# Optimization experiments

Hardware: AMD Instinct MI355X
Metric: run time of the kernel (lower is better)

Reference implementation:

```python
import jax, jax.numpy as jnp
import numpy as np

N = 50000          # nodes
E = 800000         # edges (avg degree 16)
F_IN = 64          # node feature dim
F_EDGE = 8         # edge feature dim (carried through, unused by EdgeConv)
DIMS = [64, 64, 64, 8]   # hidden layers + final num_classes layer (no BN)
EPS = 1e-5


def mish(x):
    return x * jnp.tanh(jax.nn.softplus(x))


def _init_layer(key, din, dout):
    k1, k2, k3, k4 = jax.random.split(key, 4)
    s1 = 1.0 / np.sqrt(2 * din)
    s2 = 1.0 / np.sqrt(dout)
    w1 = jax.random.uniform(k1, (2 * din, dout), jnp.float32, -s1, s1)
    b1 = jax.random.uniform(k2, (dout,), jnp.float32, -s1, s1)
    w2 = jax.random.uniform(k3, (dout, dout), jnp.float32, -s2, s2)
    b2 = jax.random.uniform(k4, (dout,), jnp.float32, -s2, s2)
    return w1, b1, w2, b2


def setup_inputs() -> dict:
    key = jax.random.key(0)
    ks = jax.random.split(key, 8)
    inp = {
        "x": jax.random.normal(ks[0], (N, F_IN), jnp.float32),
        "edge_index": jax.random.randint(ks[1], (2, E), 0, N, jnp.int32),
        "edge_attr": jax.random.normal(ks[2], (E, F_EDGE), jnp.float32),
    }
    din = F_IN
    for l, dout in enumerate(DIMS):
        w1, b1, w2, b2 = _init_layer(jax.random.fold_in(ks[3], l), din, dout)
        inp[f"w1_{l}"] = w1
        inp[f"b1_{l}"] = b1
        inp[f"w2_{l}"] = w2
        inp[f"b2_{l}"] = b2
        if l < len(DIMS) - 1:  # BN on all but final classifier layer
            inp[f"g_{l}"] = jnp.ones((dout,), jnp.float32)
            inp[f"be_{l}"] = jnp.zeros((dout,), jnp.float32)
        din = dout
    return inp


def _forward(x, edge_index, params):
    src = edge_index[0]
    dst = edge_index[1]
    for (w1, b1, w2, b2, g, be) in params:
        xi = x[dst]                       # [E, din] target feats
        xj = x[src]                       # [E, din] source feats
        m = jnp.concatenate([xi, xj - xi], axis=-1)   # [E, 2*din]
        h = mish(m @ w1 + b1) @ w2 + b2               # [E, dout]
        agg = jax.ops.segment_max(h, dst, num_segments=N)
        x = jnp.where(jnp.isfinite(agg), agg, 0.0)    # empty segments -> 0
        if g is not None:                 # BatchNorm1d, batch stats (train fwd)
            mu = x.mean(axis=0)
            var = x.var(axis=0)
            x = (x - mu) * jax.lax.rsqrt(var + EPS) * g + be
    return x


def reference(x, edge_index, edge_attr,
              w1_0, b1_0, w2_0, b2_0, g_0, be_0,
              w1_1, b1_1, w2_1, b2_1, g_1, be_1,
              w1_2, b1_2, w2_2, b2_2, g_2, be_2,
              w1_3, b1_3, w2_3, b2_3):
    params = [
        (w1_0, b1_0, w2_0, b2_0, g_0, be_0),
        (w1_1, b1_1, w2_1, b2_1, g_1, be_1),
        (w1_2, b1_2, w2_2, b2_2, g_2, be_2),
        (w1_3, b1_3, w2_3, b2_3, None, None),
    ]
    return _forward(x, edge_index, params)
```

## Files before the change

### kernel.cpp

```cpp
#include <hip/hip_runtime.h>
#include <hip/hip_bf16.h>
#include <math.h>

#define NN 50000
#define EE 800000
#define NT (EE / 16)
#define NBLK 1408
#define CHT 9

typedef short s8v __attribute__((ext_vector_type(8)));
typedef float f4v __attribute__((ext_vector_type(4)));

__device__ __forceinline__ short f2bf(float f) {
    unsigned u = __float_as_uint(f);
    u += 0x7fffu + ((u >> 16) & 1u);
    return (short)(u >> 16);
}

__device__ __forceinline__ unsigned enc(float f) {
    unsigned u = __float_as_uint(f);
    return (u & 0x80000000u) ? ~u : (u | 0x80000000u);
}
__device__ __forceinline__ float dec(unsigned k) {
    if (k == 0u) return 0.0f;
    unsigned u = (k & 0x80000000u) ? (k & 0x7fffffffu) : ~k;
    return __uint_as_float(u);
}

__device__ __forceinline__ float mish_fast(float v) {
    float t = __expf(v);
    float s = t * (t + 2.0f);
    float r = v * s * __builtin_amdgcn_rcpf(s + 2.0f);
    return (v > 15.0f) ? v : r;
}

#define MFMA16(a, b, c) __builtin_amdgcn_mfma_f32_16x16x32_bf16(a, b, c, 0, 0, 0)


__global__ __launch_bounds__(256) void count_k(const int* __restrict__ ei,
                                               int* __restrict__ cnt) {
    int e = blockIdx.x * 256 + threadIdx.x;
    if (e < EE) atomicAdd(&cnt[ei[EE + e]], 1);
}

#define NBS 196

__global__ __launch_bounds__(256) void scan_part(const int* __restrict__ cnt,
                                                 int* __restrict__ part) {
    int t = threadIdx.x, i = blockIdx.x * 256 + t;
    __shared__ int ps[256];
    ps[t] = (i < NN) ? cnt[i] : 0;
    __syncthreads();
    for (int off = 128; off > 0; off >>= 1) {
        if (t < off) ps[t] += ps[t + off];
        __syncthreads();
    }
    if (t == 0) part[blockIdx.x] = ps[0];
}

__global__ __launch_bounds__(256) void scan_top(int* __restrict__ part) {
    int t = threadIdx.x;
    int v = (t < NBS) ? part[t] : 0;
    __shared__ int ps[256];
    ps[t] = v;
    __syncthreads();
    for (int off = 1; off < 256; off <<= 1) {
        int u = (t >= off) ? ps[t - off] : 0;
        __syncthreads();
        ps[t] += u;
        __syncthreads();
    }
    if (t < NBS) part[t] = ps[t] - v;
}

__global__ __launch_bounds__(256) void scan_fin(const int* __restrict__ cnt,
                                                const int* __restrict__ part,
                                                int* __restrict__ row_off,
                                                int* __restrict__ cur) {
    int t = threadIdx.x, i = blockIdx.x * 256 + t;
    int v = (i < NN) ? cnt[i] : 0;
    __shared__ int ps[256];
    ps[t] = v;
    __syncthreads();
    for (int off = 1; off < 256; off <<= 1) {
        int u = (t >= off) ? ps[t - off] : 0;
        __syncthreads();
        ps[t] += u;
        __syncthreads();
    }
    int excl = ps[t] - v + part[blockIdx.x];
    if (i < NN) {
        row_off[i] = excl;
        cur[i] = excl;
        if (i == NN - 1) row_off[NN] = excl + v;
    }
}

__global__ __launch_bounds__(256) void scatter_k(const int* __restrict__ ei,
                                                 int* __restrict__ cur,
                                                 int* __restrict__ csr_src,
                                                 int* __restrict__ csr_dst) {
    int e = blockIdx.x * 256 + threadIdx.x;
    if (e < EE) {
        int d = ei[EE + e];
        int p = atomicAdd(&cur[d], 1);
        csr_src[p] = ei[e];
        csr_dst[p] = d;
    }
}


__global__ __launch_bounds__(256)
void cvt_bf16(const float* __restrict__ x, unsigned short* __restrict__ xb, int n) {
    int i = blockIdx.x * 256 + threadIdx.x;
    if (i < n) xb[i] = (unsigned short)f2bf(x[i]);
}


__global__ __launch_bounds__(256)
void a0_mfma(const unsigned short* __restrict__ xb, const float* __restrict__ w1,
             const float* __restrict__ b1, float* __restrict__ a0, int nwt) {
    const int lane = threadIdx.x & 63;
    const int wid = blockIdx.x * 4 + (threadIdx.x >> 6);
    const int i = lane & 15, q = lane >> 4;
    s8v wf[4][2];
#pragma unroll
    for (int nb = 0; nb < 4; nb++)
#pragma unroll
        for (int kh = 0; kh < 2; kh++)
#pragma unroll
            for (int j = 0; j < 8; j++) {
                int k = kh * 32 + q * 8 + j, n = nb * 16 + i;
                wf[nb][kh][j] = f2bf(w1[k * 64 + n] - w1[(64 + k) * 64 + n]);
            }
    float bia[4];
#pragma unroll
    for (int nb = 0; nb < 4; nb++) bia[nb] = b1[nb * 16 + i];

    const int ntiles = NN / 16;
    for (int t = wid; t < ntiles; t += nwt) {
        const int row0 = t * 16;
        const unsigned short* xr = xb + (size_t)(row0 + i) * 64;
        s8v af0 = *(const s8v*)(xr + q * 8);
        s8v af1 = *(const s8v*)(xr + 32 + q * 8);
        const int rowq = row0 + q * 4;
#pragma unroll
        for (int nb = 0; nb < 4; nb++) {
            f4v c = {0.f, 0.f, 0.f, 0.f};
            c = MFMA16(af0, wf[nb][0], c);
            c = MFMA16(af1, wf[nb][1], c);
#pragma unroll
            for (int r = 0; r < 4; r++)
                a0[(size_t)(rowq + r) * 64 + i * 4 + nb] = c[r] + bia[nb];
        }
    }
}


__global__ __launch_bounds__(256)
void a0_mfma8(const unsigned short* __restrict__ xb, const float* __restrict__ w1,
              const float* __restrict__ b1, float* __restrict__ a0, int nwt) {
    const int lane = threadIdx.x & 63;
    const int wid = blockIdx.x * 4 + (threadIdx.x >> 6);
    const int i = lane & 15, q = lane >> 4;
    s8v wf[2];
#pragma unroll
    for (int kh = 0; kh < 2; kh++)
#pragma unroll
        for (int j = 0; j < 8; j++) {
            int k = kh * 32 + q * 8 + j;
            wf[kh][j] = (i < 8) ? f2bf(w1[k * 8 + i] - w1[(64 + k) * 8 + i]) : (short)0;
        }
    const float bia = (i < 8) ? b1[i] : 0.0f;

    const int ntiles = NN / 16;
    for (int t = wid; t < ntiles; t += nwt) {
        const int row0 = t * 16;
        const unsigned short* xr = xb + (size_t)(row0 + i) * 64;
        s8v af0 = *(const s8v*)(xr + q * 8);
        s8v af1 = *(const s8v*)(xr + 32 + q * 8);
        f4v c = {0.f, 0.f, 0.f, 0.f};
        c = MFMA16(af0, wf[0], c);
        c = MFMA16(af1, wf[1], c);
        if (i < 8) {
            const int rowq = row0 + q * 4;
#pragma unroll
            for (int r = 0; r < 4; r++)
                a0[(size_t)(rowq + r) * 8 + i] = c[r] + bia;
        }
    }
}


__global__ __launch_bounds__(256)
void edge_mfma64(const unsigned short* __restrict__ xb, const float* __restrict__ a0,
                 const float* __restrict__ w1, const float* __restrict__ w2,
                 const float* __restrict__ b2,
                 const int* __restrict__ csr_src, const int* __restrict__ csr_dst,
                 unsigned* __restrict__ y) {
    __shared__ float uld[4][16 * 68];
    __shared__ int dseg[4][2][20];
    __shared__ short w2l[8 * 64 * 8];
    const int lane = threadIdx.x & 63;
    const int wv = threadIdx.x >> 6;
    const int wid = blockIdx.x * 4 + wv;
    const int i = lane & 15, q = lane >> 4;
    float* up = &uld[wv][0];

    s8v w1f[4][2];
#pragma unroll
    for (int nb = 0; nb < 4; nb++)
#pragma unroll
        for (int kh = 0; kh < 2; kh++)
#pragma unroll
            for (int j = 0; j < 8; j++) {
                int k = kh * 32 + q * 8 + j, n = nb * 16 + i;
                w1f[nb][kh][j] = f2bf(w1[(64 + k) * 64 + n]);
            }
    {
        const int nb = wv;
#pragma unroll
        for (int kh = 0; kh < 2; kh++) {
            s8v uu;
#pragma unroll
            for (int j = 0; j < 8; j++) {
                int k = kh * 32 + q * 8 + j;
                uu[j] = f2bf(w2[k * 64 + nb * 16 + i]);
            }
            *(s8v*)(w2l + ((nb * 2 + kh) * 64 + lane) * 8) = uu;
        }
    }
    __syncthreads();

    const float b2c = b2[lane];

    int t = wid * CHT;
    if (t >= NT) return;
    const int tend = (t + CHT < NT) ? (t + CHT) : NT;

    s8v af0_c, af1_c;
    {
        int s0 = csr_src[t * 16 + i];
        const unsigned short* xr = xb + (size_t)s0 * 64;
        af0_c = *(const s8v*)(xr + q * 8);
        af1_c = *(const s8v*)(xr + 32 + q * 8);
    }
    int src_n = (t + 1 < tend) ? csr_src[(t + 1) * 16 + i] : 0;
    if (lane < 17) {
        int e = t * 16 + lane;
        dseg[wv][t & 1][lane] = (e < EE) ? csr_dst[e] : -1;
    }
    asm volatile("s_waitcnt lgkmcnt(0)" ::: "memory");
    int dq_c[4];
#pragma unroll
    for (int r = 0; r < 4; r++) dq_c[r] = dseg[wv][t & 1][q * 4 + r];
    f4v a0r_c[4];
#pragma unroll
    for (int r = 0; r < 4; r++)
        a0r_c[r] = *(const f4v*)(a0 + (size_t)dq_c[r] * 64 + i * 4);

    float run = -INFINITY;

    for (; t < tend; t++) {
        const bool has_n = (t + 1) < tend;
        int* dsg = &dseg[wv][t & 1][0];
        int* dsg_n = &dseg[wv][(t + 1) & 1][0];

        if (has_n && lane < 17) {
            int e = (t + 1) * 16 + lane;
            dsg_n[lane] = (e < EE) ? csr_dst[e] : -1;
        }
        s8v af0_n = {0,0,0,0,0,0,0,0}, af1_n = {0,0,0,0,0,0,0,0};
        if (has_n) {
            const unsigned short* xr = xb + (size_t)src_n * 64;
            af0_n = *(const s8v*)(xr + q * 8);
            af1_n = *(const s8v*)(xr + 32 + q * 8);
        }
        int src_nn = (t + 2 < tend) ? csr_src[(t + 2) * 16 + i] : 0;

        f4v c0 = {0.f, 0.f, 0.f, 0.f}, c1 = c0, c2 = c0, c3 = c0;
        c0 = MFMA16(af0_c, w1f[0][0], c0); c0 = MFMA16(af1_c, w1f[0][1], c0);
        c1 = MFMA16(af0_c, w1f[1][0], c1); c1 = MFMA16(af1_c, w1f[1][1], c1);
        c2 = MFMA16(af0_c, w1f[2][0], c2); c2 = MFMA16(af1_c, w1f[2][1], c2);
        c3 = MFMA16(af0_c, w1f[3][0], c3); c3 = MFMA16(af1_c, w1f[3][1], c3);

        asm volatile("" ::: "memory");
#pragma unroll
        for (int r = 0; r < 4; r++) {
            const int ro = (q * 4 + r) * 68 + i;
            up[ro +  0] = mish_fast(c0[r] + a0r_c[r][0]);
            up[ro + 16] = mish_fast(c1[r] + a0r_c[r][1]);
            up[ro + 32] = mish_fast(c2[r] + a0r_c[r][2]);
            up[ro + 48] = mish_fast(c3[r] + a0r_c[r][3]);
        }
        asm volatile("s_waitcnt lgkmcnt(0)" ::: "memory");

        int dq_n[4];
        f4v a0r_n[4];
        if (has_n) {
#pragma unroll
            for (int r = 0; r < 4; r++) dq_n[r] = dsg_n[q * 4 + r];
#pragma unroll
            for (int r = 0; r < 4; r++)
                a0r_n[r] = *(const f4v*)(a0 + (size_t)dq_n[r] * 64 + i * 4);
        }

        s8v uf[2];
#pragma unroll
        for (int kh = 0; kh < 2; kh++) {
            const f4v* rp = (const f4v*)(up + i * 68 + kh * 32 + q * 8);
            f4v v0 = rp[0], v1 = rp[1];
            s8v uu;
            uu[0] = f2bf(v0[0]); uu[1] = f2bf(v0[1]);
            uu[2] = f2bf(v0[2]); uu[3] = f2bf(v0[3]);
            uu[4] = f2bf(v1[0]); uu[5] = f2bf(v1[1]);
            uu[6] = f2bf(v1[2]); uu[7] = f2bf(v1[3]);
            uf[kh] = uu;
        }
        asm volatile("" ::: "memory");

        f4v cc[4];
#pragma unroll
        for (int nb = 0; nb < 4; nb++) {
            s8v b0 = *(const s8v*)(w2l + ((nb * 2 + 0) * 64 + lane) * 8);
            s8v b1v = *(const s8v*)(w2l + ((nb * 2 + 1) * 64 + lane) * 8);
            f4v c = {0.f, 0.f, 0.f, 0.f};
            c = MFMA16(uf[0], b0, c);
            c = MFMA16(uf[1], b1v, c);
            cc[nb] = c;
        }

#pragma unroll
        for (int nb = 0; nb < 4; nb++)
#pragma unroll
            for (int r = 0; r < 4; r++)
                up[(q * 4 + r) * 68 + nb * 16 + i] = cc[nb][r];
        asm volatile("s_waitcnt lgkmcnt(0)" ::: "memory");

        float v[16];
#pragma unroll
        for (int row = 0; row < 16; row++) v[row] = up[row * 68 + lane];

        int dcur = dsg[0];
#pragma unroll
        for (int row = 0; row < 16; row++) {
            run = fmaxf(run, v[row]);
            int dn = (row < 15) ? dsg[row + 1] : (has_n ? dsg[16] : -1);
            if (dcur != dn) {
                atomicMax(&y[(size_t)dcur * 64 + lane], enc(run + b2c));
                run = -INFINITY;
            }
            dcur = dn;
        }
        asm volatile("s_waitcnt lgkmcnt(0)" ::: "memory");

        src_n = src_nn;
        af0_c = af0_n; af1_c = af1_n;
#pragma unroll
        for (int r = 0; r < 4; r++) a0r_c[r] = a0r_n[r];
    }
}


__global__ __launch_bounds__(256)
void edge_mfma16(const unsigned short* __restrict__ xb, const float* __restrict__ a0,
                 const float* __restrict__ w1, const float* __restrict__ w2,
                 const float* __restrict__ b2,
                 const int* __restrict__ csr_src, const int* __restrict__ csr_dst,
                 unsigned* __restrict__ y8) {
    __shared__ float uld[4][16 * 20];
    __shared__ int dseg[4][2][20];
    const int lane = threadIdx.x & 63;
    const int wv = threadIdx.x >> 6;
    const int wid = blockIdx.x * 4 + wv;
    const int i = lane & 15, q = lane >> 4;
    float* up = &uld[wv][0];

    s8v w1f[2], w2f;
#pragma unroll
    for (int kh = 0; kh < 2; kh++)
#pragma unroll
        for (int j = 0; j < 8; j++) {
            int k = kh * 32 + q * 8 + j;
            w1f[kh][j] = (i < 8) ? f2bf(w1[(64 + k) * 8 + i]) : (short)0;
        }
#pragma unroll
    for (int j = 0; j < 8; j++)
        w2f[j] = (q == 0 && i < 8) ? f2bf(w2[j * 8 + i]) : (short)0;
    const float b2c = (lane < 8) ? b2[lane] : 0.0f;

    int t = wid * CHT;
    if (t >= NT) return;
    const int tend = (t + CHT < NT) ? (t + CHT) : NT;

    s8v af0_c, af1_c;
    {
        int s0 = csr_src[t * 16 + i];
        const unsigned short* xr = xb + (size_t)s0 * 64;
        af0_c = *(const s8v*)(xr + q * 8);
        af1_c = *(const s8v*)(xr + 32 + q * 8);
    }
    int src_n = (t + 1 < tend) ? csr_src[(t + 1) * 16 + i] : 0;
    if (lane < 17) {
        int e = t * 16 + lane;
        dseg[wv][t & 1][lane] = (e < EE) ? csr_dst[e] : -1;
    }
    asm volatile("s_waitcnt lgkmcnt(0)" ::: "memory");
    int dq_c[4];
#pragma unroll
    for (int r = 0; r < 4; r++) dq_c[r] = dseg[wv][t & 1][q * 4 + r];
    float av_c[4];
#pragma unroll
    for (int r = 0; r < 4; r++)
        av_c[r] = (i < 8) ? a0[(size_t)dq_c[r] * 8 + i] : 0.0f;

    float run = -INFINITY;

    for (; t < tend; t++) {
        const bool has_n = (t + 1) < tend;
        int* dsg = &dseg[wv][t & 1][0];
        int* dsg_n = &dseg[wv][(t + 1) & 1][0];

        if (has_n && lane < 17) {
            int e = (t + 1) * 16 + lane;
            dsg_n[lane] = (e < EE) ? csr_dst[e] : -1;
        }
        s8v af0_n = {0,0,0,0,0,0,0,0}, af1_n = {0,0,0,0,0,0,0,0};
        if (has_n) {
            const unsigned short* xr = xb + (size_t)src_n * 64;
            af0_n = *(const s8v*)(xr + q * 8);
            af1_n = *(const s8v*)(xr + 32 + q * 8);
        }
        int src_nn = (t + 2 < tend) ? csr_src[(t + 2) * 16 + i] : 0;

        f4v c = {0.f, 0.f, 0.f, 0.f};
        c = MFMA16(af0_c, w1f[0], c);
        c = MFMA16(af1_c, w1f[1], c);

        asm volatile("" ::: "memory");
#pragma unroll
        for (int r = 0; r < 4; r++)
            up[(q * 4 + r) * 20 + i] = mish_fast(c[r] + av_c[r]);
        asm volatile("s_waitcnt lgkmcnt(0)" ::: "memory");

        int dq_n[4];
        float av_n[4] = {0, 0, 0, 0};
        if (has_n) {
#pragma unroll
            for (int r = 0; r < 4; r++) dq_n[r] = dsg_n[q * 4 + r];
#pragma unroll
            for (int r = 0; r < 4; r++)
                av_n[r] = (i < 8) ? a0[(size_t)dq_n[r] * 8 + i] : 0.0f;
        }

        s8v uf = {0,0,0,0,0,0,0,0};
        if (q < 2) {
            const f4v* rp = (const f4v*)(up + i * 20 + q * 8);
            f4v v0 = rp[0], v1 = rp[1];
            uf[0] = f2bf(v0[0]); uf[1] = f2bf(v0[1]);
            uf[2] = f2bf(v0[2]); uf[3] = f2bf(v0[3]);
            uf[4] = f2bf(v1[0]); uf[5] = f2bf(v1[1]);
            uf[6] = f2bf(v1[2]); uf[7] = f2bf(v1[3]);
        }
        asm volatile("" ::: "memory");

        f4v cc = {0.f, 0.f, 0.f, 0.f};
        cc = MFMA16(uf, w2f, cc);

#pragma unroll
        for (int r = 0; r < 4; r++)
            up[(q * 4 + r) * 20 + i] = cc[r];
        asm volatile("s_waitcnt lgkmcnt(0)" ::: "memory");

        float v[16];
#pragma unroll
        for (int row = 0; row < 16; row++) v[row] = up[row * 20 + (lane & 7)];

        int dcur = dsg[0];
#pragma unroll
        for (int row = 0; row < 16; row++) {
            run = fmaxf(run, v[row]);
            int dn = (row < 15) ? dsg[row + 1] : (has_n ? dsg[16] : -1);
            if (dcur != dn) {
                if (lane < 8)
                    atomicMax(&y8[(size_t)dcur * 8 + lane], enc(run + b2c));
                run = -INFINITY;
            }
            dcur = dn;
        }
        asm volatile("s_waitcnt lgkmcnt(0)" ::: "memory");

        src_n = src_nn;
        af0_c = af0_n; af1_c = af1_n;
#pragma unroll
        for (int r = 0; r < 4; r++) av_c[r] = av_n[r];
    }
}


__global__ __launch_bounds__(256)
void bn_stats(const unsigned* __restrict__ yk, float* __restrict__ st) {
    const int tid = threadIdx.x;
    const int ch = tid & 63, grp = tid >> 6;
    float s = 0, qq = 0;
    for (int n = blockIdx.x * 4 + grp; n < NN; n += gridDim.x * 4) {
        float v = dec(yk[(size_t)n * 64 + ch]);
        s += v;
        qq = fmaf(v, v, qq);
    }
    __shared__ float ls[256], lq[256];
    ls[tid] = s; lq[tid] = qq;
    __syncthreads();
    if (tid < 64) {
        s  = ls[tid] + ls[tid + 64] + ls[tid + 128] + ls[tid + 192];
        qq = lq[tid] + lq[tid + 64] + lq[tid + 128] + lq[tid + 192];
        atomicAdd(&st[ch], s);
        atomicAdd(&st[64 + ch], qq);
    }
}

__global__ __launch_bounds__(256)
void bn_apply(unsigned* __restrict__ yk, const float* __restrict__ st,
              const float* __restrict__ g, const float* __restrict__ be,
              unsigned short* __restrict__ xbout) {
    int idx = blockIdx.x * 256 + threadIdx.x;
    if (idx >= NN * 64) return;
    int ch = idx & 63;
    float mu  = st[ch] * (1.0f / NN);
    float var = st[64 + ch] * (1.0f / NN) - mu * mu;
    float sc  = rsqrtf(var + 1e-5f) * g[ch];
    float v = (dec(yk[idx]) - mu) * sc + be[ch];
    xbout[idx] = (unsigned short)f2bf(v);
    yk[idx] = 0u;
}

__global__ __launch_bounds__(256)
void decode_out(const unsigned* __restrict__ y8, float* __restrict__ out) {
    int idx = blockIdx.x * 256 + threadIdx.x;
    if (idx < NN * 8) out[idx] = dec(y8[idx]);
}


extern "C" void kernel_launch(void* const* d_in, const int* in_sizes, int n_in,
                              void* d_out, int out_size, void* d_ws, size_t ws_size,
                              hipStream_t stream) {
    const float* x0 = (const float*)d_in[0];
    const int*   ei = (const int*)d_in[1];
    const float* w1[4] = {(const float*)d_in[3],  (const float*)d_in[9],
                          (const float*)d_in[15], (const float*)d_in[21]};
    const float* b1[4] = {(const float*)d_in[4],  (const float*)d_in[10],
                          (const float*)d_in[16], (const float*)d_in[22]};
    const float* w2[4] = {(const float*)d_in[5],  (const float*)d_in[11],
                          (const float*)d_in[17], (const float*)d_in[23]};
    const float* b2[4] = {(const float*)d_in[6],  (const float*)d_in[12],
                          (const float*)d_in[18], (const float*)d_in[24]};
    const float* gg[3] = {(const float*)d_in[7],  (const float*)d_in[13],
                          (const float*)d_in[19]};
    const float* be[3] = {(const float*)d_in[8],  (const float*)d_in[14],
                          (const float*)d_in[20]};

    char* p = (char*)d_ws;
    auto alloc = [&](size_t bytes) -> char* {
        char* r = p;
        p += (bytes + 255) & ~(size_t)255;
        return r;
    };
    int*      cnt     = (int*)alloc((size_t)NN * 4);
    int*      part    = (int*)alloc((size_t)NBS * 4);
    int*      row_off = (int*)alloc((size_t)(NN + 1) * 4);
    int*      cur     = (int*)alloc((size_t)NN * 4);
    int*      csr_s   = (int*)alloc((size_t)EE * 4);
    int*      csr_d   = (int*)alloc((size_t)EE * 4);
    float*    st      = (float*)alloc(3 * 128 * 4);
    float*    a0      = (float*)alloc((size_t)NN * 64 * 4);
    unsigned* y       = (unsigned*)alloc((size_t)NN * 64 * 4);
    unsigned* y8      = (unsigned*)alloc((size_t)NN * 8 * 4);
    unsigned short* xb0 = (unsigned short*)alloc((size_t)NN * 64 * 2);
    unsigned short* xbA = (unsigned short*)alloc((size_t)NN * 64 * 2);
    unsigned short* xbB = xb0;

    hipMemsetAsync(cnt, 0, (size_t)NN * 4, stream);
    hipMemsetAsync(st, 0, 3 * 128 * 4, stream);
    hipMemsetAsync(y, 0, (size_t)NN * 64 * 4, stream);
    hipMemsetAsync(y8, 0, (size_t)NN * 8 * 4, stream);

    count_k<<<(EE + 255) / 256, 256, 0, stream>>>(ei, cnt);
    scan_part<<<NBS, 256, 0, stream>>>(cnt, part);
    scan_top<<<1, 256, 0, stream>>>(part);
    scan_fin<<<NBS, 256, 0, stream>>>(cnt, part, row_off, cur);
    scatter_k<<<(EE + 255) / 256, 256, 0, stream>>>(ei, cur, csr_s, csr_d);
    cvt_bf16<<<(NN * 64 + 255) / 256, 256, 0, stream>>>(x0, xb0, NN * 64);

    const int NBA = 256;
    const int NWA = NBA * 4;

    const unsigned short* xin[3] = {xb0, xbA, xbB};
    unsigned short* xout[3] = {xbA, xbB, xbA};
    for (int l = 0; l < 3; l++) {
        a0_mfma<<<NBA, 256, 0, stream>>>(xin[l], w1[l], b1[l], a0, NWA);
        edge_mfma64<<<NBLK, 256, 0, stream>>>(xin[l], a0, w1[l], w2[l], b2[l],
                                              csr_s, csr_d, y);
        bn_stats<<<256, 256, 0, stream>>>(y, st + 128 * l);
        bn_apply<<<(NN * 64 + 255) / 256, 256, 0, stream>>>(y, st + 128 * l,
                                                            gg[l], be[l], xout[l]);
    }

    a0_mfma8<<<NBA, 256, 0, stream>>>(xbA, w1[3], b1[3], a0, NWA);
    edge_mfma16<<<NBLK, 256, 0, stream>>>(xbA, a0, w1[3], w2[3], b2[3],
                                          csr_s, csr_d, y8);
    decode_out<<<(NN * 8 + 255) / 256, 256, 0, stream>>>(y8, (float*)d_out);
}
```

Baseline: 547.6 us.

## Fuse BN apply with next-layer node projection and bf16 conversion

Merges the float-to-bf16 conversion with the first per-node projection kernel, and folds the y/y8 zeroing into it instead of using memsets. It also merges the BatchNorm apply step with the next layer's node-side MFMA projection, so normalized features feed the projection directly from registers. This removes several kernel launches and an extra read and write of the bf16 node features per layer. In exchange each fused kernel does more work per tile, with a fixed grid of 196 blocks.

```diff
diff --git a/kernel.cpp b/kernel.cpp
--- a/kernel.cpp
+++ b/kernel.cpp
@@ -7,6 +7,9 @@
 #define NT (EE / 16)
 #define NBLK 1408
 #define CHT 9
+#define NTN (NN / 16)
+#define NBF 196
+#define NWF (NBF * 4)
 
 typedef short s8v __attribute__((ext_vector_type(8)));
 typedef float f4v __attribute__((ext_vector_type(4)));
@@ -111,17 +114,13 @@
 
 
 __global__ __launch_bounds__(256)
-void cvt_bf16(const float* __restrict__ x, unsigned short* __restrict__ xb, int n) {
-    int i = blockIdx.x * 256 + threadIdx.x;
-    if (i < n) xb[i] = (unsigned short)f2bf(x[i]);
-}
-
-
-__global__ __launch_bounds__(256)
-void a0_mfma(const unsigned short* __restrict__ xb, const float* __restrict__ w1,
-             const float* __restrict__ b1, float* __restrict__ a0, int nwt) {
-    const int lane = threadIdx.x & 63;
-    const int wid = blockIdx.x * 4 + (threadIdx.x >> 6);
+void cvt_a0(const float* __restrict__ x, const float* __restrict__ w1,
+            const float* __restrict__ b1, unsigned short* __restrict__ xb,
+            float* __restrict__ a0, unsigned* __restrict__ y,
+            unsigned* __restrict__ y8) {
+    const int tid = threadIdx.x;
+    const int lane = tid & 63;
+    const int wid = blockIdx.x * 4 + (tid >> 6);
     const int i = lane & 15, q = lane >> 4;
     s8v wf[4][2];
 #pragma unroll
@@ -137,13 +136,21 @@
 #pragma unroll
     for (int nb = 0; nb < 4; nb++) bia[nb] = b1[nb * 16 + i];
 
-    const int ntiles = NN / 16;
-    for (int t = wid; t < ntiles; t += nwt) {
-        const int row0 = t * 16;
-        const unsigned short* xr = xb + (size_t)(row0 + i) * 64;
-        s8v af0 = *(const s8v*)(xr + q * 8);
-        s8v af1 = *(const s8v*)(xr + 32 + q * 8);
-        const int rowq = row0 + q * 4;
+    for (int t = wid; t < NTN; t += NWF) {
+        const int row = t * 16 + i;
+        const float* xr = x + (size_t)row * 64 + q * 8;
+        f4v x0 = *(const f4v*)xr,        x1 = *(const f4v*)(xr + 4);
+        f4v x2 = *(const f4v*)(xr + 32), x3 = *(const f4v*)(xr + 36);
+        s8v af0, af1;
+#pragma unroll
+        for (int j = 0; j < 4; j++) {
+            af0[j] = f2bf(x0[j]); af0[4 + j] = f2bf(x1[j]);
+            af1[j] = f2bf(x2[j]); af1[4 + j] = f2bf(x3[j]);
+        }
+        unsigned short* xw = xb + (size_t)row * 64 + q * 8;
+        *(s8v*)xw = af0;
+        *(s8v*)(xw + 32) = af1;
+        const int rowq = t * 16 + q * 4;
 #pragma unroll
         for (int nb = 0; nb < 4; nb++) {
             f4v c = {0.f, 0.f, 0.f, 0.f};
@@ -154,39 +161,163 @@
                 a0[(size_t)(rowq + r) * 64 + i * 4 + nb] = c[r] + bia[nb];
         }
     }
+    const int gt = blockIdx.x * 256 + tid, gs = NBF * 256;
+    for (int idx = gt; idx < NN * 64; idx += gs) y[idx] = 0u;
+    for (int idx = gt; idx < NN * 8; idx += gs) y8[idx] = 0u;
 }
 
 
 __global__ __launch_bounds__(256)
-void a0_mfma8(const unsigned short* __restrict__ xb, const float* __restrict__ w1,
-              const float* __restrict__ b1, float* __restrict__ a0, int nwt) {
-    const int lane = threadIdx.x & 63;
-    const int wid = blockIdx.x * 4 + (threadIdx.x >> 6);
+void bn_a0_64(unsigned* __restrict__ yk, const float* __restrict__ st,
+              const float* __restrict__ g, const float* __restrict__ be,
+              const float* __restrict__ w1n, const float* __restrict__ b1n,
+              unsigned short* __restrict__ xbout, float* __restrict__ a0out) {
+    __shared__ float sa[64], sb[64];
+    const int tid = threadIdx.x;
+    if (tid < 64) {
+        float mu  = st[tid] * (1.0f / NN);
+        float var = st[64 + tid] * (1.0f / NN) - mu * mu;
+        float sc  = rsqrtf(var + 1e-5f) * g[tid];
+        sa[tid] = sc;
+        sb[tid] = be[tid] - mu * sc;
+    }
+    __syncthreads();
+    const int lane = tid & 63;
+    const int wid = blockIdx.x * 4 + (tid >> 6);
     const int i = lane & 15, q = lane >> 4;
+
+    s8v wf[4][2];
+#pragma unroll
+    for (int nb = 0; nb < 4; nb++)
+#pragma unroll
+        for (int kh = 0; kh < 2; kh++)
+#pragma unroll
+            for (int j = 0; j < 8; j++) {
+                int k = kh * 32 + q * 8 + j, n = nb * 16 + i;
+                wf[nb][kh][j] = f2bf(w1n[k * 64 + n] - w1n[(64 + k) * 64 + n]);
+            }
+    float bia[4];
+#pragma unroll
+    for (int nb = 0; nb < 4; nb++) bia[nb] = b1n[nb * 16 + i];
+
+    f4v a00 = *(const f4v*)(sa + q * 8),      a01 = *(const f4v*)(sa + q * 8 + 4);
+    f4v a10 = *(const f4v*)(sa + 32 + q * 8), a11 = *(const f4v*)(sa + 36 + q * 8);
+    f4v b00 = *(const f4v*)(sb + q * 8),      b01 = *(const f4v*)(sb + q * 8 + 4);
+    f4v b10 = *(const f4v*)(sb + 32 + q * 8), b11 = *(const f4v*)(sb + 36 + q * 8);
+
+    const uint4 z4 = {0u, 0u, 0u, 0u};
+    for (int t = wid; t < NTN; t += NWF) {
+        const int row = t * 16 + i;
+        unsigned* yr = yk + (size_t)row * 64 + q * 8;
+        uint4 u0 = *(const uint4*)yr,        u1 = *(const uint4*)(yr + 4);
+        uint4 u2 = *(const uint4*)(yr + 32), u3 = *(const uint4*)(yr + 36);
+        s8v af0, af1;
+        af0[0] = f2bf(dec(u0.x) * a00[0] + b00[0]);
+        af0[1] = f2bf(dec(u0.y) * a00[1] + b00[1]);
+        af0[2] = f2bf(dec(u0.z) * a00[2] + b00[2]);
+        af0[3] = f2bf(dec(u0.w) * a00[3] + b00[3]);
+        af0[4] = f2bf(dec(u1.x) * a01[0] + b01[0]);
+        af0[5] = f2bf(dec(u1.y) * a01[1] + b01[1]);
+        af0[6] = f2bf(dec(u1.z) * a01[2] + b01[2]);
+        af0[7] = f2bf(dec(u1.w) * a01[3] + b01[3]);
+        af1[0] = f2bf(dec(u2.x) * a10[0] + b10[0]);
+        af1[1] = f2bf(dec(u2.y) * a10[1] + b10[1]);
+        af1[2] = f2bf(dec(u2.z) * a10[2] + b10[2]);
+        af1[3] = f2bf(dec(u2.w) * a10[3] + b10[3]);
+        af1[4] = f2bf(dec(u3.x) * a11[0] + b11[0]);
+        af1[5] = f2bf(dec(u3.y) * a11[1] + b11[1]);
+        af1[6] = f2bf(dec(u3.z) * a11[2] + b11[2]);
+        af1[7] = f2bf(dec(u3.w) * a11[3] + b11[3]);
+
+        unsigned short* xw = xbout + (size_t)row * 64 + q * 8;
+        *(s8v*)xw = af0;
+        *(s8v*)(xw + 32) = af1;
+        *(uint4*)yr = z4;        *(uint4*)(yr + 4) = z4;
+        *(uint4*)(yr + 32) = z4; *(uint4*)(yr + 36) = z4;
+
+        const int rowq = t * 16 + q * 4;
+#pragma unroll
+        for (int nb = 0; nb < 4; nb++) {
+            f4v c = {0.f, 0.f, 0.f, 0.f};
+            c = MFMA16(af0, wf[nb][0], c);
+            c = MFMA16(af1, wf[nb][1], c);
+#pragma unroll
+            for (int r = 0; r < 4; r++)
+                a0out[(size_t)(rowq + r) * 64 + i * 4 + nb] = c[r] + bia[nb];
+        }
+    }
+}
+
+
+__global__ __launch_bounds__(256)
+void bn_a0_8(unsigned* __restrict__ yk, const float* __restrict__ st,
+             const float* __restrict__ g, const float* __restrict__ be,
+             const float* __restrict__ w1n, const float* __restrict__ b1n,
+             unsigned short* __restrict__ xbout, float* __restrict__ a08) {
+    __shared__ float sa[64], sb[64];
+    const int tid = threadIdx.x;
+    if (tid < 64) {
+        float mu  = st[tid] * (1.0f / NN);
+        float var = st[64 + tid] * (1.0f / NN) - mu * mu;
+        float sc  = rsqrtf(var + 1e-5f) * g[tid];
+        sa[tid] = sc;
+        sb[tid] = be[tid] - mu * sc;
+    }
+    __syncthreads();
+    const int lane = tid & 63;
+    const int wid = blockIdx.x * 4 + (tid >> 6);
+    const int i = lane & 15, q = lane >> 4;
+
     s8v wf[2];
 #pragma unroll
     for (int kh = 0; kh < 2; kh++)
 #pragma unroll
         for (int j = 0; j < 8; j++) {
             int k = kh * 32 + q * 8 + j;
-            wf[kh][j] = (i < 8) ? f2bf(w1[k * 8 + i] - w1[(64 + k) * 8 + i]) : (short)0;
-        }
-    const float bia = (i < 8) ? b1[i] : 0.0f;
-
-    const int ntiles = NN / 16;
-    for (int t = wid; t < ntiles; t += nwt) {
-        const int row0 = t * 16;
-        const unsigned short* xr = xb + (size_t)(row0 + i) * 64;
-        s8v af0 = *(const s8v*)(xr + q * 8);
-        s8v af1 = *(const s8v*)(xr + 32 + q * 8);
+            wf[kh][j] = (i < 8) ? f2bf(w1n[k * 8 + i] - w1n[(64 + k) * 8 + i]) : (short)0;
+        }
+    const float bia = (i < 8) ? b1n[i] : 0.0f;
+
+    f4v a00 = *(const f4v*)(sa + q * 8),      a01 = *(const f4v*)(sa + q * 8 + 4);
+    f4v a10 = *(const f4v*)(sa + 32 + q * 8), a11 = *(const f4v*)(sa + 36 + q * 8);
+    f4v b00 = *(const f4v*)(sb + q * 8),      b01 = *(const f4v*)(sb + q * 8 + 4);
+    f4v b10 = *(const f4v*)(sb + 32 + q * 8), b11 = *(const f4v*)(sb + 36 + q * 8);
+
+    for (int t = wid; t < NTN; t += NWF) {
+        const int row = t * 16 + i;
+        const unsigned* yr = yk + (size_t)row * 64 + q * 8;
+        uint4 u0 = *(const uint4*)yr,        u1 = *(const uint4*)(yr + 4);
+        uint4 u2 = *(const uint4*)(yr + 32), u3 = *(const uint4*)(yr + 36);
+        s8v af0, af1;
+        af0[0] = f2bf(dec(u0.x) * a00[0] + b00[0]);
+        af0[1] = f2bf(dec(u0.y) * a00[1] + b00[1]);
+        af0[2] = f2bf(dec(u0.z) * a00[2] + b00[2]);
+        af0[3] = f2bf(dec(u0.w) * a00[3] + b00[3]);
+        af0[4] = f2bf(dec(u1.x) * a01[0] + b01[0]);
+        af0[5] = f2bf(dec(u1.y) * a01[1] + b01[1]);
+        af0[6] = f2bf(dec(u1.z) * a01[2] + b01[2]);
+        af0[7] = f2bf(dec(u1.w) * a01[3] + b01[3]);
+        af1[0] = f2bf(dec(u2.x) * a10[0] + b10[0]);
+        af1[1] = f2bf(dec(u2.y) * a10[1] + b10[1]);
+        af1[2] = f2bf(dec(u2.z) * a10[2] + b10[2]);
+        af1[3] = f2bf(dec(u2.w) * a10[3] + b10[3]);
+        af1[4] = f2bf(dec(u3.x) * a11[0] + b11[0]);
+        af1[5] = f2bf(dec(u3.y) * a11[1] + b11[1]);
+        af1[6] = f2bf(dec(u3.z) * a11[2] + b11[2]);
+        af1[7] = f2bf(dec(u3.w) * a11[3] + b11[3]);
+
+        unsigned short* xw = xbout + (size_t)row * 64 + q * 8;
+        *(s8v*)xw = af0;
+        *(s8v*)(xw + 32) = af1;
+
         f4v c = {0.f, 0.f, 0.f, 0.f};
         c = MFMA16(af0, wf[0], c);
         c = MFMA16(af1, wf[1], c);
         if (i < 8) {
-            const int rowq = row0 + q * 4;
+            const int rowq = t * 16 + q * 4;
 #pragma unroll
             for (int r = 0; r < 4; r++)
-                a0[(size_t)(rowq + r) * 8 + i] = c[r] + bia;
+                a08[(size_t)(rowq + r) * 8 + i] = c[r] + bia;
         }
     }
 }
@@ -517,21 +648,6 @@
         atomicAdd(&st[ch], s);
         atomicAdd(&st[64 + ch], qq);
     }
-}
-
-__global__ __launch_bounds__(256)
-void bn_apply(unsigned* __restrict__ yk, const float* __restrict__ st,
-              const float* __restrict__ g, const float* __restrict__ be,
-              unsigned short* __restrict__ xbout) {
-    int idx = blockIdx.x * 256 + threadIdx.x;
-    if (idx >= NN * 64) return;
-    int ch = idx & 63;
-    float mu  = st[ch] * (1.0f / NN);
-    float var = st[64 + ch] * (1.0f / NN) - mu * mu;
-    float sc  = rsqrtf(var + 1e-5f) * g[ch];
-    float v = (dec(yk[idx]) - mu) * sc + be[ch];
-    xbout[idx] = (unsigned short)f2bf(v);
-    yk[idx] = 0u;
 }
 
 __global__ __launch_bounds__(256)
@@ -581,31 +697,30 @@
 
     hipMemsetAsync(cnt, 0, (size_t)NN * 4, stream);
     hipMemsetAsync(st, 0, 3 * 128 * 4, stream);
-    hipMemsetAsync(y, 0, (size_t)NN * 64 * 4, stream);
-    hipMemsetAsync(y8, 0, (size_t)NN * 8 * 4, stream);
 
     count_k<<<(EE + 255) / 256, 256, 0, stream>>>(ei, cnt);
     scan_part<<<NBS, 256, 0, stream>>>(cnt, part);
     scan_top<<<1, 256, 0, stream>>>(part);
     scan_fin<<<NBS, 256, 0, stream>>>(cnt, part, row_off, cur);
     scatter_k<<<(EE + 255) / 256, 256, 0, stream>>>(ei, cur, csr_s, csr_d);
-    cvt_bf16<<<(NN * 64 + 255) / 256, 256, 0, stream>>>(x0, xb0, NN * 64);
-
-    const int NBA = 256;
-    const int NWA = NBA * 4;
-
-    const unsigned short* xin[3] = {xb0, xbA, xbB};
-    unsigned short* xout[3] = {xbA, xbB, xbA};
-    for (int l = 0; l < 3; l++) {
-        a0_mfma<<<NBA, 256, 0, stream>>>(xin[l], w1[l], b1[l], a0, NWA);
-        edge_mfma64<<<NBLK, 256, 0, stream>>>(xin[l], a0, w1[l], w2[l], b2[l],
-                                              csr_s, csr_d, y);
-        bn_stats<<<256, 256, 0, stream>>>(y, st + 128 * l);
-        bn_apply<<<(NN * 64 + 255) / 256, 256, 0, stream>>>(y, st + 128 * l,
-                                                            gg[l], be[l], xout[l]);
-    }
-
-    a0_mfma8<<<NBA, 256, 0, stream>>>(xbA, w1[3], b1[3], a0, NWA);
+
+    cvt_a0<<<NBF, 256, 0, stream>>>(x0, w1[0], b1[0], xb0, a0, y, y8);
+
+    edge_mfma64<<<NBLK, 256, 0, stream>>>(xb0, a0, w1[0], w2[0], b2[0],
+                                          csr_s, csr_d, y);
+    bn_stats<<<256, 256, 0, stream>>>(y, st);
+    bn_a0_64<<<NBF, 256, 0, stream>>>(y, st, gg[0], be[0], w1[1], b1[1], xbA, a0);
+
+    edge_mfma64<<<NBLK, 256, 0, stream>>>(xbA, a0, w1[1], w2[1], b2[1],
+                                          csr_s, csr_d, y);
+    bn_stats<<<256, 256, 0, stream>>>(y, st + 128);
+    bn_a0_64<<<NBF, 256, 0, stream>>>(y, st + 128, gg[1], be[1], w1[2], b1[2], xbB, a0);
+
+    edge_mfma64<<<NBLK, 256, 0, stream>>>(xbB, a0, w1[2], w2[2], b2[2],
+                                          csr_s, csr_d, y);
+    bn_stats<<<256, 256, 0, stream>>>(y, st + 256);
+    bn_a0_8<<<NBF, 256, 0, stream>>>(y, st + 256, gg[2], be[2], w1[3], b1[3], xbA, a0);
+
     edge_mfma16<<<NBLK, 256, 0, stream>>>(xbA, a0, w1[3], w2[3], b2[3],
                                           csr_s, csr_d, y8);
     decode_out<<<(NN * 8 + 255) / 256, 256, 0, stream>>>(y8, (float*)d_out);
```

Result: no change. 541.6 us (-1.1%).
